# Kernel tuning notes

Hardware: AMD Instinct MI355X
Metric: run time of the kernel (lower is better)

The kernel has to match this reference:

```python
import jax, jax.numpy as jnp
import numpy as np

SOS_TOKEN = 0


def setup_inputs() -> dict:
    key = jax.random.key(0)
    ks = jax.random.split(key, 16)
    B, S, T, H, V = 64, 64, 32, 512, 32000
    s = 1.0 / np.sqrt(H)
    inp = {
        "encoder_outputs": jax.random.normal(ks[0], (B, S, H), jnp.float32),
        "encoder_hidden": jax.random.normal(ks[1], (1, B, H), jnp.float32),
        "target_tensor": jax.random.randint(ks[2], (B, T), 0, V),
        "emb": jax.random.normal(ks[3], (V, H), jnp.float32),
        "Wa": jax.random.uniform(ks[4], (H, H), jnp.float32, -s, s),
        "ba": jnp.zeros((H,), jnp.float32),
        "Ua": jax.random.uniform(ks[5], (H, H), jnp.float32, -s, s),
        "bu": jnp.zeros((H,), jnp.float32),
        "va": jax.random.uniform(ks[6], (H, 1), jnp.float32, -s, s),
        "bv": jnp.zeros((1,), jnp.float32),
        "w_ih": jax.random.uniform(ks[7], (3 * H, 2 * H), jnp.float32, -s, s),
        "b_ih": jax.random.uniform(ks[8], (3 * H,), jnp.float32, -s, s),
        "w_hh": jax.random.uniform(ks[9], (3 * H, H), jnp.float32, -s, s),
        "b_hh": jax.random.uniform(ks[10], (3 * H,), jnp.float32, -s, s),
        "Wo": jax.random.uniform(ks[11], (V, H), jnp.float32, -s, s),
        "bo": jax.random.uniform(ks[12], (V,), jnp.float32, -s, s),
    }
    return inp


def _gru_cell(x, h, w_ih, b_ih, w_hh, b_hh):
    # x: [B, 2H], h: [B, H] -- PyTorch nn.GRU gate math
    H = h.shape[-1]
    gi = x @ w_ih.T + b_ih            # [B, 3H]
    gh = h @ w_hh.T + b_hh            # [B, 3H]
    i_r, i_z, i_n = gi[:, :H], gi[:, H:2 * H], gi[:, 2 * H:]
    h_r, h_z, h_n = gh[:, :H], gh[:, H:2 * H], gh[:, 2 * H:]
    r = jax.nn.sigmoid(i_r + h_r)
    z = jax.nn.sigmoid(i_z + h_z)
    n = jnp.tanh(i_n + r * h_n)
    return (1.0 - z) * n + z * h


def reference(encoder_outputs, encoder_hidden, target_tensor,
              emb, Wa, ba, Ua, bu, va, bv,
              w_ih, b_ih, w_hh, b_hh, Wo, bo):
    B, S, H = encoder_outputs.shape
    T = target_tensor.shape[1]
    # Teacher forcing: step t input is SOS for t=0 else target[:, t-1]
    sos = jnp.full((B, 1), SOS_TOKEN, dtype=target_tensor.dtype)
    input_ids = jnp.concatenate([sos, target_tensor[:, :-1]], axis=1)  # [B, T]
    embedded = emb[input_ids]  # [B, T, H]  (dropout is identity in eval)

    # Precompute key projection once (invariant across steps)
    Ua_keys = encoder_outputs @ Ua.T + bu  # [B, S, H]

    def step(h, x_emb):
        # Bahdanau additive attention: query = hidden state
        scores = jnp.tanh(h[:, None, :] @ Wa.T + ba + Ua_keys) @ va + bv  # [B, S, 1]
        scores = scores[..., 0]                                           # [B, S]
        attn = jax.nn.softmax(scores, axis=-1)
        context = jnp.einsum('bs,bsh->bh', attn, encoder_outputs)
        x = jnp.concatenate([x_emb, context], axis=-1)                    # [B, 2H]
        h_new = _gru_cell(x, h, w_ih, b_ih, w_hh, b_hh)
        logits = h_new @ Wo.T + bo                                        # [B, V]
        return h_new, (logits, attn)

    h0 = encoder_hidden[0]  # [B, H]
    h_final, (logits_t, attn_t) = jax.lax.scan(step, h0, jnp.swapaxes(embedded, 0, 1))
    logits = jnp.swapaxes(logits_t, 0, 1)        # [B, T, V]
    attentions = jnp.swapaxes(attn_t, 0, 1)      # [B, T, S]
    log_probs = jax.nn.log_softmax(logits, axis=-1)
    decoder_hidden = h_final[None]               # [1, B, H]
    return (log_probs, decoder_hidden, attentions)
```

## Files before the change

kernel.cpp:

```cpp
#include <hip/hip_runtime.h>

typedef unsigned short u16;
typedef __bf16 bf16x8 __attribute__((ext_vector_type(8)));
typedef float f32x4 __attribute__((ext_vector_type(4)));

#define Bsz 64
#define Ssz 64
#define Tsz 32
#define Hsz 512
#define Vsz 32000
#define NCONV 160
#define NTOT 256

static __device__ inline u16 f2bf(float f) {
    union { float f; unsigned u; } v; v.f = f;
    unsigned u = v.u;
    unsigned r = (u + 0x7FFFu + ((u >> 16) & 1u)) >> 16;
    return (u16)r;
}
static __device__ inline float bf2f(u16 v) {
    union { unsigned u; float f; } x; x.u = ((unsigned)v) << 16; return x.f;
}
static __device__ inline float tanh_fast(float x) {
    float e = __expf(2.f * x);
    return 1.f - 2.f / (e + 1.f);
}
static __device__ inline void st_u32(unsigned* p, unsigned v) {
    __hip_atomic_store(p, v, __ATOMIC_RELAXED, __HIP_MEMORY_SCOPE_AGENT);
}
static __device__ inline unsigned ld_u32(const unsigned* p) {
    return __hip_atomic_load(p, __ATOMIC_RELAXED, __HIP_MEMORY_SCOPE_AGENT);
}

#define GLOAD_LDS16(g, l) \
    __builtin_amdgcn_global_load_lds((const __attribute__((address_space(1))) void*)(g), \
                                     (__attribute__((address_space(3))) void*)(l), 16, 0, 0)

__global__ void prep_kernel(const float* __restrict__ enc, const float* __restrict__ Ua,
                            const float* __restrict__ Wa, const float* __restrict__ wih,
                            const float* __restrict__ whh, const float* __restrict__ ehid,
                            u16* __restrict__ encbf, u16* __restrict__ Uabf,
                            u16* __restrict__ Wabf, u16* __restrict__ wihbf,
                            u16* __restrict__ whhbf, u16* __restrict__ h0bf) {
    const int n0 = 2097152, n1 = 262144, n2 = 262144, n3 = 1572864, n4 = 786432, n5 = 32768;
    const int total = n0 + n1 + n2 + n3 + n4 + n5;
    for (int i = blockIdx.x * blockDim.x + threadIdx.x; i < total; i += gridDim.x * blockDim.x) {
        int j = i;
        if (j < n0) { encbf[j] = f2bf(enc[j]); continue; } j -= n0;
        if (j < n1) { Uabf[j] = f2bf(Ua[j]); continue; } j -= n1;
        if (j < n2) { Wabf[j] = f2bf(Wa[j]); continue; } j -= n2;
        if (j < n3) { wihbf[j] = f2bf(wih[j]); continue; } j -= n3;
        if (j < n4) { whhbf[j] = f2bf(whh[j]); continue; } j -= n4;
        h0bf[j] = f2bf(ehid[j]);
    }
}

__global__ void embed_kernel(const int* __restrict__ target, const float* __restrict__ emb,
                             u16* __restrict__ xbuf) {
    int n = Tsz * Bsz * Hsz;
    for (int i = blockIdx.x * blockDim.x + threadIdx.x; i < n; i += gridDim.x * blockDim.x) {
        int t = i / (Bsz * Hsz);
        int rem = i % (Bsz * Hsz);
        int b = rem / Hsz, k = rem % Hsz;
        int id = (t == 0) ? 0 : target[b * Tsz + (t - 1)];
        xbuf[((size_t)t * Bsz + b) * 1024 + k] = f2bf(emb[(size_t)id * Hsz + k]);
    }
}

__global__ __launch_bounds__(256) void gemm_bt(const u16* __restrict__ A, const u16* __restrict__ Bw,
                                               const float* __restrict__ bias, float* __restrict__ out,
                                               int M, int N, int K) {
    __shared__ __align__(16) u16 As[128 * 32];
    __shared__ __align__(16) u16 Bs[128 * 32];
    int m0 = blockIdx.x * 128, n0 = blockIdx.y * 128;
    int tid = threadIdx.x, lane = tid & 63, wid = tid >> 6;
    int wm = wid & 1, wn = wid >> 1;
    f32x4 acc[4][4] = {};
    for (int k0 = 0; k0 < K; k0 += 32) {
        int e0 = wid * 64 + lane;
        int e1 = e0 + 256;
        GLOAD_LDS16(&A[(size_t)(m0 + (e0 >> 2)) * K + k0 + (e0 & 3) * 8], (char*)As + wid * 1024);
        GLOAD_LDS16(&A[(size_t)(m0 + (e1 >> 2)) * K + k0 + (e1 & 3) * 8], (char*)As + 4096 + wid * 1024);
        GLOAD_LDS16(&Bw[(size_t)(n0 + (e0 >> 2)) * K + k0 + (e0 & 3) * 8], (char*)Bs + wid * 1024);
        GLOAD_LDS16(&Bw[(size_t)(n0 + (e1 >> 2)) * K + k0 + (e1 & 3) * 8], (char*)Bs + 4096 + wid * 1024);
        __syncthreads();
        bf16x8 av[4], bvv[4];
        for (int mi = 0; mi < 4; ++mi)
            av[mi] = *(const bf16x8*)&As[(wm * 64 + mi * 16 + (lane & 15)) * 32 + (lane >> 4) * 8];
        for (int ni = 0; ni < 4; ++ni)
            bvv[ni] = *(const bf16x8*)&Bs[(wn * 64 + ni * 16 + (lane & 15)) * 32 + (lane >> 4) * 8];
        for (int mi = 0; mi < 4; ++mi)
            for (int ni = 0; ni < 4; ++ni)
                acc[mi][ni] = __builtin_amdgcn_mfma_f32_16x16x32_bf16(av[mi], bvv[ni], acc[mi][ni], 0, 0, 0);
        __syncthreads();
    }
    for (int mi = 0; mi < 4; ++mi)
        for (int ni = 0; ni < 4; ++ni) {
            int n = n0 + wn * 64 + ni * 16 + (lane & 15);
            float bb = bias[n];
            for (int r = 0; r < 4; ++r) {
                int m = m0 + wm * 64 + mi * 16 + (lane >> 4) * 4 + r;
                out[(size_t)m * N + n] = acc[mi][ni][r] + bb;
            }
        }
}

static __device__ inline void arrive(unsigned* bar, int slot, unsigned val, int tid) {
    asm volatile("s_waitcnt vmcnt(0)" ::: "memory");
    __syncthreads();
    if (tid == 0) st_u32(&bar[slot * 32], val);
}
static __device__ inline void pollflags(unsigned* bar, int base, int n, unsigned target, int tid) {
    if (tid < n) {
        unsigned* p = &bar[(base + tid) * 32];
        while (ld_u32(p) < target) {}
    }
    __syncthreads();
}

__global__ __launch_bounds__(512, 1) void coop_kernel(
    const float* __restrict__ uak,
    u16* __restrict__ xbuf, u16* __restrict__ Abf,
    const u16* __restrict__ h0bf, const u16* __restrict__ wihbf, const u16* __restrict__ whhbf,
    const u16* __restrict__ Wabf, const float* __restrict__ enc,
    const float* __restrict__ va, const float* __restrict__ bv, const float* __restrict__ ba,
    const float* __restrict__ b_ih, const float* __restrict__ b_hh,
    const float* __restrict__ ehid,
    const float* __restrict__ Wo, u16* __restrict__ Wobf,
    float* __restrict__ out, u16* __restrict__ partials,
    unsigned* __restrict__ bar) {
    __shared__ __align__(16) char lds[149504];
    __shared__ float WhL[512];
    __shared__ float scL[64];
    __shared__ float vaL[512];

    const size_t HID_OFF = (size_t)Bsz * Tsz * Vsz;
    const size_t ATT_OFF = HID_OFF + (size_t)Bsz * Hsz;

    int tid = threadIdx.x, lane = tid & 63, wid = tid >> 6;
    int ln15 = lane & 15, hi = lane >> 4;
    int bx = blockIdx.x;

    unsigned* xbufU = (unsigned*)xbuf;
    unsigned* AbfU = (unsigned*)Abf;
    unsigned* partU = (unsigned*)partials;

    if (bx < 64) {
        int b = bx;
        u16* uakL = (u16*)lds;
        u16* encL = (u16*)(lds + 65536);
        for (int i = tid; i < Ssz * Hsz; i += 512) {
            uakL[i] = f2bf(uak[(size_t)b * Ssz * Hsz + i]);
            encL[i] = f2bf(enc[(size_t)b * Ssz * Hsz + i]);
        }
        vaL[tid] = va[tid];
        float bvv = bv[0];
        float ba_t = ba[tid];
        int halfsel = tid & 1;
        __syncthreads();

        for (int t = 0; t < Tsz; ++t) {
            pollflags(bar, 64, 32, (unsigned)(t + 1), tid);
            {
                float acc = ba_t;
                const unsigned* pb = partU + (size_t)b * 256 + (tid >> 1);
#pragma unroll
                for (int g = 0; g < 32; ++g) {
                    unsigned pw = ld_u32(pb + (size_t)g * 16384);
                    acc += bf2f((u16)(halfsel ? (pw >> 16) : (pw & 0xffff)));
                }
                WhL[tid] = acc;
            }
            __syncthreads();
            for (int si = 0; si < 8; ++si) {
                int s = wid * 8 + si;
                float a = 0.f;
#pragma unroll
                for (int ji = 0; ji < 8; ++ji) {
                    int j = lane + ji * 64;
                    float x = WhL[j] + bf2f(uakL[s * 512 + j]);
                    a += tanh_fast(x) * vaL[j];
                }
                for (int off = 32; off; off >>= 1) a += __shfl_down(a, off);
                if (lane == 0) scL[s] = a + bvv;
            }
            __syncthreads();
            if (wid == 0) {
                float x = scL[lane];
                float mx = x;
                for (int off = 32; off; off >>= 1) mx = fmaxf(mx, __shfl_xor(mx, off));
                float e = __expf(x - mx);
                float sm = e;
                for (int off = 32; off; off >>= 1) sm += __shfl_xor(sm, off);
                float at = e / sm;
                scL[lane] = at;
                out[ATT_OFF + ((size_t)b * Tsz + t) * Ssz + lane] = at;
            }
            __syncthreads();
            float c = 0.f;
            for (int s = 0; s < Ssz; ++s)
                c += scL[s] * bf2f(encL[s * 512 + tid]);
            unsigned me = (unsigned)f2bf(c);
            unsigned other = __shfl_xor(me, 1);
            if ((tid & 1) == 0)
                st_u32(&xbufU[((size_t)t * Bsz + b) * 512 + 256 + (tid >> 1)], me | (other << 16));
            arrive(bar, bx, (unsigned)(t + 1), tid);
        }
    } else if (bx < 96) {
        int g = bx - 64, jbase = g * 16;
        u16* hsl = (u16*)(lds + 147456);
        for (int i = tid; i < 6144; i += 512) {
            int row = i >> 7, c16 = i & 127;
            int Rg = (row >> 4) * 512 + jbase + (row & 15);
            uint4 v = *(const uint4*)&wihbf[(size_t)Rg * 1024 + c16 * 8];
            *(uint4*)(lds + row * 2048 + ((c16 * 16) ^ ((row & 7) << 4))) = v;
        }
        for (int i = tid; i < 3072; i += 512) {
            int row = i >> 6, c16 = i & 63;
            int Rg = (row >> 4) * 512 + jbase + (row & 15);
            uint4 v = *(const uint4*)&whhbf[(size_t)Rg * 512 + c16 * 8];
            *(uint4*)(lds + 98304 + row * 1024 + ((c16 * 16) ^ ((row & 7) << 4))) = v;
        }
        const char* wih_l = lds;
        const char* whh_l = lds + 98304;
        int j = jbase + ln15;
        float bir = b_ih[j] + b_hh[j];
        float biz = b_ih[512 + j] + b_hh[512 + j];
        float bin = b_ih[1024 + j];
        float bhn = b_hh[1024 + j];
        float hp0 = 0.f, hp1 = 0.f, hp2 = 0.f, hp3 = 0.f;
        if (wid < 4) {
            int m = wid;
            hp0 = ehid[(size_t)(m * 16 + hi * 4 + 0) * Hsz + j];
            hp1 = ehid[(size_t)(m * 16 + hi * 4 + 1) * Hsz + j];
            hp2 = ehid[(size_t)(m * 16 + hi * 4 + 2) * Hsz + j];
            hp3 = ehid[(size_t)(m * 16 + hi * 4 + 3) * Hsz + j];
        }
        int swz = (ln15 & 7) << 4;
        bf16x8 zfr = {};
        bf16x8 wfrag[4];
#pragma unroll
        for (int i = 0; i < 4; ++i) {
            int jp = (wid * 4 + i) * 16 + ln15;
            wfrag[i] = (hi < 2) ? *(const bf16x8*)&Wabf[(size_t)jp * 512 + jbase + hi * 8] : zfr;
        }
        for (int i = tid; i < 1024; i += 512)
            hsl[i] = h0bf[(size_t)(i >> 4) * 512 + jbase + (i & 15)];
        __syncthreads();
#pragma unroll
        for (int mt = 0; mt < 4; ++mt) {
            bf16x8 af = (hi < 2) ? *(const bf16x8*)&hsl[(mt * 16 + ln15) * 16 + hi * 8] : zfr;
#pragma unroll
            for (int i = 0; i < 4; ++i) {
                f32x4 pacc = {};
                pacc = __builtin_amdgcn_mfma_f32_16x16x32_bf16(af, wfrag[i], pacc, 0, 0, 0);
                int n0 = (wid * 4 + i) * 16;
#pragma unroll
                for (int r = 0; r < 4; ++r) {
                    int b = mt * 16 + hi * 4 + r;
                    unsigned me = (unsigned)f2bf(pacc[r]);
                    unsigned other = __shfl_xor(me, 1);
                    if ((ln15 & 1) == 0)
                        st_u32(&partU[((size_t)g * 64 + b) * 256 + ((n0 + ln15) >> 1)], me | (other << 16));
                }
            }
        }
        arrive(bar, bx, 1u, tid);

        for (int t = 0; t < Tsz; ++t) {
            const u16* hbt = t ? (Abf + (size_t)(t - 1) * Bsz * Hsz) : h0bf;
            pollflags(bar, 64, 32, (unsigned)(t + 1), tid);
            f32x4 ar = {}, az = {}, ain = {}, ahn = {};
            if (wid < 4) {
                int m = wid;
#pragma unroll 8
                for (int k0 = 0; k0 < 16; ++k0) {
                    bf16x8 a = *(const bf16x8*)&xbuf[((size_t)t * Bsz + m * 16 + ln15) * 1024 + k0 * 32 + hi * 8];
                    int byteIn = k0 * 64 + hi * 16;
                    bf16x8 b0 = *(const bf16x8*)(wih_l + (0 + ln15) * 2048 + (byteIn ^ swz));
                    bf16x8 b1 = *(const bf16x8*)(wih_l + (16 + ln15) * 2048 + (byteIn ^ swz));
                    bf16x8 b2 = *(const bf16x8*)(wih_l + (32 + ln15) * 2048 + (byteIn ^ swz));
                    ar = __builtin_amdgcn_mfma_f32_16x16x32_bf16(a, b0, ar, 0, 0, 0);
                    az = __builtin_amdgcn_mfma_f32_16x16x32_bf16(a, b1, az, 0, 0, 0);
                    ain = __builtin_amdgcn_mfma_f32_16x16x32_bf16(a, b2, ain, 0, 0, 0);
                }
#pragma unroll 8
                for (int k0 = 0; k0 < 16; ++k0) {
                    bf16x8 a = *(const bf16x8*)&hbt[(size_t)(m * 16 + ln15) * 512 + k0 * 32 + hi * 8];
                    int byteIn = k0 * 64 + hi * 16;
                    bf16x8 b0 = *(const bf16x8*)(whh_l + (0 + ln15) * 1024 + (byteIn ^ swz));
                    bf16x8 b1 = *(const bf16x8*)(whh_l + (16 + ln15) * 1024 + (byteIn ^ swz));
                    bf16x8 b2 = *(const bf16x8*)(whh_l + (32 + ln15) * 1024 + (byteIn ^ swz));
                    ar = __builtin_amdgcn_mfma_f32_16x16x32_bf16(a, b0, ar, 0, 0, 0);
                    az = __builtin_amdgcn_mfma_f32_16x16x32_bf16(a, b1, az, 0, 0, 0);
                    ahn = __builtin_amdgcn_mfma_f32_16x16x32_bf16(a, b2, ahn, 0, 0, 0);
                }
                unsigned* p = &bar[(wid * 16 + ln15) * 32];
                while (ld_u32(p) < (unsigned)(t + 1)) {}
#pragma unroll 8
                for (int k0 = 16; k0 < 32; ++k0) {
                    bf16x8 a = *(const bf16x8*)&xbuf[((size_t)t * Bsz + m * 16 + ln15) * 1024 + k0 * 32 + hi * 8];
                    int byteIn = k0 * 64 + hi * 16;
                    bf16x8 b0 = *(const bf16x8*)(wih_l + (0 + ln15) * 2048 + (byteIn ^ swz));
                    bf16x8 b1 = *(const bf16x8*)(wih_l + (16 + ln15) * 2048 + (byteIn ^ swz));
                    bf16x8 b2 = *(const bf16x8*)(wih_l + (32 + ln15) * 2048 + (byteIn ^ swz));
                    ar = __builtin_amdgcn_mfma_f32_16x16x32_bf16(a, b0, ar, 0, 0, 0);
                    az = __builtin_amdgcn_mfma_f32_16x16x32_bf16(a, b1, az, 0, 0, 0);
                    ain = __builtin_amdgcn_mfma_f32_16x16x32_bf16(a, b2, ain, 0, 0, 0);
                }
                float hpv[4] = {hp0, hp1, hp2, hp3};
#pragma unroll
                for (int r = 0; r < 4; ++r) {
                    int b = m * 16 + hi * 4 + r;
                    float rg = 1.f / (1.f + __expf(-(ar[r] + bir)));
                    float zg = 1.f / (1.f + __expf(-(az[r] + biz)));
                    float ng = tanh_fast(ain[r] + bin + rg * (ahn[r] + bhn));
                    float hv = (1.f - zg) * ng + zg * hpv[r];
                    hpv[r] = hv;
                    u16 hb = f2bf(hv);
                    unsigned me = (unsigned)hb;
                    unsigned other = __shfl_xor(me, 1);
                    if ((ln15 & 1) == 0)
                        st_u32(&AbfU[((size_t)t * Bsz + b) * 256 + (j >> 1)], me | (other << 16));
                    hsl[b * 16 + ln15] = hb;
                    if (t == Tsz - 1) out[HID_OFF + (size_t)b * 512 + j] = hv;
                }
                hp0 = hpv[0]; hp1 = hpv[1]; hp2 = hpv[2]; hp3 = hpv[3];
            }
            __syncthreads();
#pragma unroll
            for (int mt = 0; mt < 4; ++mt) {
                bf16x8 af = (hi < 2) ? *(const bf16x8*)&hsl[(mt * 16 + ln15) * 16 + hi * 8] : zfr;
#pragma unroll
                for (int i = 0; i < 4; ++i) {
                    f32x4 pacc = {};
                    pacc = __builtin_amdgcn_mfma_f32_16x16x32_bf16(af, wfrag[i], pacc, 0, 0, 0);
                    int n0 = (wid * 4 + i) * 16;
#pragma unroll
                    for (int r = 0; r < 4; ++r) {
                        int b = mt * 16 + hi * 4 + r;
                        unsigned me = (unsigned)f2bf(pacc[r]);
                        unsigned other = __shfl_xor(me, 1);
                        if ((ln15 & 1) == 0)
                            st_u32(&partU[((size_t)g * 64 + b) * 256 + ((n0 + ln15) >> 1)], me | (other << 16));
                    }
                }
            }
            arrive(bar, bx, (unsigned)(t + 2), tid);
        }
    } else {
        const float4* W4 = (const float4*)Wo;
        for (int i = (bx - 96) * 512 + tid; i < (Vsz * Hsz) / 4; i += NCONV * 512) {
            float4 v = W4[i];
            ushort4 o;
            o.x = f2bf(v.x); o.y = f2bf(v.y); o.z = f2bf(v.z); o.w = f2bf(v.w);
            *(ushort4*)&Wobf[(size_t)i * 4] = o;
        }
    }
}

static __device__ inline void l_stage(const u16* __restrict__ Abf, const u16* __restrict__ Wobf,
                                      int m0, int n0, int k0, char* As, char* Bs, int wid, int lane) {
    int e0 = wid * 64 + lane;
    int r = e0 >> 2, c8 = (e0 & 3) * 8;
    GLOAD_LDS16(&Abf[(size_t)(m0 + r) * 512 + k0 + c8], As + wid * 1024);
    GLOAD_LDS16(&Wobf[(size_t)(n0 + r) * 512 + k0 + c8], Bs + wid * 1024);
    GLOAD_LDS16(&Wobf[(size_t)(n0 + 128 + r) * 512 + k0 + c8], Bs + 8192 + wid * 1024);
}

__global__ __launch_bounds__(512) void gemm_logits(const u16* __restrict__ Abf, const u16* __restrict__ Wobf,
                                                   const float* __restrict__ bo, float* __restrict__ out,
                                                   float* __restrict__ sumexp) {
    __shared__ __align__(16) char lds[49152];
    char* As0 = lds;
    char* Bs0 = lds + 8192;
    char* As1 = lds + 24576;
    char* Bs1 = lds + 32768;
    int tid = threadIdx.x, lane = tid & 63, wid = tid >> 6;
    int ln15 = lane & 15, hi = lane >> 4;
    int wm = wid & 1, wn = wid >> 1;
    int job = blockIdx.x;
    int m0 = (job / 125) * 128, n0 = (job % 125) * 256;
    f32x4 acc[4][4] = {};
    l_stage(Abf, Wobf, m0, n0, 0, As0, Bs0, wid, lane);
#pragma unroll 2
    for (int ks = 0; ks < 16; ++ks) {
        const u16* As = (const u16*)((ks & 1) ? As1 : As0);
        const u16* Bs = (const u16*)((ks & 1) ? Bs1 : Bs0);
        if (ks < 15) {
            l_stage(Abf, Wobf, m0, n0, (ks + 1) * 32,
                    (ks & 1) ? As0 : As1, (ks & 1) ? Bs0 : Bs1, wid, lane);
            asm volatile("s_waitcnt vmcnt(3)" ::: "memory");
        } else {
            asm volatile("s_waitcnt vmcnt(0)" ::: "memory");
        }
        __builtin_amdgcn_s_barrier();
        bf16x8 av[4], bvv[4];
        for (int mi = 0; mi < 4; ++mi)
            av[mi] = *(const bf16x8*)&As[(wm * 64 + mi * 16 + ln15) * 32 + hi * 8];
        for (int ni = 0; ni < 4; ++ni)
            bvv[ni] = *(const bf16x8*)&Bs[(wn * 64 + ni * 16 + ln15) * 32 + hi * 8];
        for (int mi = 0; mi < 4; ++mi)
            for (int ni = 0; ni < 4; ++ni)
                acc[mi][ni] = __builtin_amdgcn_mfma_f32_16x16x32_bf16(av[mi], bvv[ni], acc[mi][ni], 0, 0, 0);
        asm volatile("s_waitcnt lgkmcnt(0)" ::: "memory");
        __builtin_amdgcn_s_barrier();
    }
    float rowpart[4][4];
    for (int mi = 0; mi < 4; ++mi)
        for (int r = 0; r < 4; ++r) rowpart[mi][r] = 0.f;
    for (int mi = 0; mi < 4; ++mi)
        for (int ni = 0; ni < 4; ++ni) {
            int n = n0 + wn * 64 + ni * 16 + ln15;
            float bb = bo[n];
            for (int r = 0; r < 4; ++r) {
                int m = m0 + wm * 64 + mi * 16 + hi * 4 + r;
                int t = m >> 6, b = m & 63;
                float val = acc[mi][ni][r] + bb;
                out[((size_t)(b * Tsz + t)) * Vsz + n] = val;
                rowpart[mi][r] += __expf(val);
            }
        }
    for (int mi = 0; mi < 4; ++mi)
        for (int r = 0; r < 4; ++r) {
            float v = rowpart[mi][r];
            v += __shfl_xor(v, 1);
            v += __shfl_xor(v, 2);
            v += __shfl_xor(v, 4);
            v += __shfl_xor(v, 8);
            if (ln15 == 0) {
                int m = m0 + wm * 64 + mi * 16 + hi * 4 + r;
                atomicAdd(&sumexp[(m & 63) * Tsz + (m >> 6)], v);
            }
        }
}

__global__ void sub_kernel(float* __restrict__ out, const float* __restrict__ sumexp) {
    const int total4 = (Bsz * Tsz * Vsz) / 4;
    float4* o4 = (float4*)out;
    for (int i = blockIdx.x * blockDim.x + threadIdx.x; i < total4; i += gridDim.x * blockDim.x) {
        float l = __logf(sumexp[i / (Vsz / 4)]);
        float4 v = o4[i];
        v.x -= l; v.y -= l; v.z -= l; v.w -= l;
        o4[i] = v;
    }
}

extern "C" void kernel_launch(void* const* d_in, const int* in_sizes, int n_in,
                              void* d_out, int out_size, void* d_ws, size_t ws_size,
                              hipStream_t stream) {
    const float* enc   = (const float*)d_in[0];
    const float* ehid  = (const float*)d_in[1];
    const int*   target= (const int*)d_in[2];
    const float* emb   = (const float*)d_in[3];
    const float* Wa    = (const float*)d_in[4];
    const float* ba    = (const float*)d_in[5];
    const float* Ua    = (const float*)d_in[6];
    const float* bu    = (const float*)d_in[7];
    const float* va    = (const float*)d_in[8];
    const float* bv    = (const float*)d_in[9];
    const float* w_ih  = (const float*)d_in[10];
    const float* b_ih  = (const float*)d_in[11];
    const float* w_hh  = (const float*)d_in[12];
    const float* b_hh  = (const float*)d_in[13];
    const float* Wo    = (const float*)d_in[14];
    const float* bo    = (const float*)d_in[15];
    float* out = (float*)d_out;

    char* w = (char*)d_ws;
    float* uak    = (float*)w; w += (size_t)4096 * 512 * 4;
    float* sumexp = (float*)w; w += 8192;
    unsigned* bar = (unsigned*)w; w += 96 * 128;
    u16* xbuf     = (u16*)w;   w += (size_t)Tsz * Bsz * 1024 * 2;
    u16* Abf      = (u16*)w;   w += (size_t)Tsz * Bsz * Hsz * 2;
    u16* h0bf     = (u16*)w;   w += (size_t)Bsz * Hsz * 2;
    u16* partials = (u16*)w;   w += (size_t)32 * Bsz * Hsz * 2;
    u16* Wabf     = (u16*)w;   w += (size_t)Hsz * Hsz * 2;
    u16* encbf    = (u16*)w;   w += (size_t)4096 * 512 * 2;
    u16* Uabf     = (u16*)w;   w += (size_t)Hsz * Hsz * 2;
    u16* wihbf    = (u16*)w;   w += (size_t)1536 * 1024 * 2;
    u16* whhbf    = (u16*)w;   w += (size_t)1536 * 512 * 2;
    u16* Wobf     = (u16*)w;   w += (size_t)Vsz * 512 * 2;

    prep_kernel<<<2048, 256, 0, stream>>>(enc, Ua, Wa, w_ih, w_hh, ehid,
                                          encbf, Uabf, Wabf, wihbf, whhbf, h0bf);
    embed_kernel<<<1024, 256, 0, stream>>>(target, emb, xbuf);

    gemm_bt<<<dim3(32, 4), 256, 0, stream>>>(encbf, Uabf, bu, uak, 4096, 512, 512);

    hipMemsetAsync(bar, 0, 96 * 128, stream);
    hipMemsetAsync(sumexp, 0, 2048 * 4, stream);

    coop_kernel<<<NTOT, 512, 0, stream>>>(uak, xbuf, Abf, h0bf, wihbf, whhbf,
                                          Wabf, enc, va, bv, ba, b_ih, b_hh,
                                          ehid, Wo, Wobf, out, partials, bar);

    gemm_logits<<<2000, 512, 0, stream>>>(Abf, Wobf, bo, out, sumexp);

    sub_kernel<<<2048, 256, 0, stream>>>(out, sumexp);
}
```

Baseline: 976.4 us.

## Fuse embed into prep, sleep in spin-waits, move poll, coalesce logits epilogue

Folds the embedding gather into the prep conversion kernel to drop one launch. Adds s_sleep to spin-wait loops, which cuts memory traffic from polling. Moves the barrier poll in the GRU blocks after the input-side MFMAs so that work overlaps the wait. Rewrites the logits epilogue to stage each tile through LDS, giving coalesced float4 stores and one wavefront reduction per row for the sum of exponentials. The sleep can add wake-up latency on the critical recurrent path.

After: 844.9 us. 1.16x faster.

```diff
diff --git a/kernel.cpp b/kernel.cpp
--- a/kernel.cpp
+++ b/kernel.cpp
@@ -39,11 +39,14 @@
 __global__ void prep_kernel(const float* __restrict__ enc, const float* __restrict__ Ua,
                             const float* __restrict__ Wa, const float* __restrict__ wih,
                             const float* __restrict__ whh, const float* __restrict__ ehid,
+                            const int* __restrict__ target, const float* __restrict__ emb,
                             u16* __restrict__ encbf, u16* __restrict__ Uabf,
                             u16* __restrict__ Wabf, u16* __restrict__ wihbf,
-                            u16* __restrict__ whhbf, u16* __restrict__ h0bf) {
+                            u16* __restrict__ whhbf, u16* __restrict__ h0bf,
+                            u16* __restrict__ xbuf) {
     const int n0 = 2097152, n1 = 262144, n2 = 262144, n3 = 1572864, n4 = 786432, n5 = 32768;
-    const int total = n0 + n1 + n2 + n3 + n4 + n5;
+    const int n6 = Tsz * Bsz * Hsz;
+    const int total = n0 + n1 + n2 + n3 + n4 + n5 + n6;
     for (int i = blockIdx.x * blockDim.x + threadIdx.x; i < total; i += gridDim.x * blockDim.x) {
         int j = i;
         if (j < n0) { encbf[j] = f2bf(enc[j]); continue; } j -= n0;
@@ -51,19 +54,14 @@
         if (j < n2) { Wabf[j] = f2bf(Wa[j]); continue; } j -= n2;
         if (j < n3) { wihbf[j] = f2bf(wih[j]); continue; } j -= n3;
         if (j < n4) { whhbf[j] = f2bf(whh[j]); continue; } j -= n4;
-        h0bf[j] = f2bf(ehid[j]);
-    }
-}
-
-__global__ void embed_kernel(const int* __restrict__ target, const float* __restrict__ emb,
-                             u16* __restrict__ xbuf) {
-    int n = Tsz * Bsz * Hsz;
-    for (int i = blockIdx.x * blockDim.x + threadIdx.x; i < n; i += gridDim.x * blockDim.x) {
-        int t = i / (Bsz * Hsz);
-        int rem = i % (Bsz * Hsz);
-        int b = rem / Hsz, k = rem % Hsz;
-        int id = (t == 0) ? 0 : target[b * Tsz + (t - 1)];
-        xbuf[((size_t)t * Bsz + b) * 1024 + k] = f2bf(emb[(size_t)id * Hsz + k]);
+        if (j < n5) { h0bf[j] = f2bf(ehid[j]); continue; } j -= n5;
+        {
+            int t = j / (Bsz * Hsz);
+            int rem = j % (Bsz * Hsz);
+            int b = rem / Hsz, k = rem % Hsz;
+            int id = (t == 0) ? 0 : target[b * Tsz + (t - 1)];
+            xbuf[((size_t)t * Bsz + b) * 1024 + k] = f2bf(emb[(size_t)id * Hsz + k]);
+        }
     }
 }
 
@@ -110,10 +108,10 @@
     __syncthreads();
     if (tid == 0) st_u32(&bar[slot * 32], val);
 }
-static __device__ inline void pollflags(unsigned* bar, int base, int n, unsigned target, int tid) {
+static __device__ inline void pollflags1(unsigned* bar, int base, int n, unsigned target, int tid) {
     if (tid < n) {
         unsigned* p = &bar[(base + tid) * 32];
-        while (ld_u32(p) < target) {}
+        while (ld_u32(p) < target) asm volatile("s_sleep 1");
     }
     __syncthreads();
 }
@@ -160,7 +158,7 @@
         __syncthreads();
 
         for (int t = 0; t < Tsz; ++t) {
-            pollflags(bar, 64, 32, (unsigned)(t + 1), tid);
+            pollflags1(bar, 64, 32, (unsigned)(t + 1), tid);
             {
                 float acc = ba_t;
                 const unsigned* pb = partU + (size_t)b * 256 + (tid >> 1);
@@ -269,7 +267,6 @@
 
         for (int t = 0; t < Tsz; ++t) {
             const u16* hbt = t ? (Abf + (size_t)(t - 1) * Bsz * Hsz) : h0bf;
-            pollflags(bar, 64, 32, (unsigned)(t + 1), tid);
             f32x4 ar = {}, az = {}, ain = {}, ahn = {};
             if (wid < 4) {
                 int m = wid;
@@ -284,6 +281,10 @@
                     az = __builtin_amdgcn_mfma_f32_16x16x32_bf16(a, b1, az, 0, 0, 0);
                     ain = __builtin_amdgcn_mfma_f32_16x16x32_bf16(a, b2, ain, 0, 0, 0);
                 }
+            }
+            pollflags1(bar, 64, 32, (unsigned)(t + 1), tid);
+            if (wid < 4) {
+                int m = wid;
 #pragma unroll 8
                 for (int k0 = 0; k0 < 16; ++k0) {
                     bf16x8 a = *(const bf16x8*)&hbt[(size_t)(m * 16 + ln15) * 512 + k0 * 32 + hi * 8];
@@ -296,7 +297,7 @@
                     ahn = __builtin_amdgcn_mfma_f32_16x16x32_bf16(a, b2, ahn, 0, 0, 0);
                 }
                 unsigned* p = &bar[(wid * 16 + ln15) * 32];
-                while (ld_u32(p) < (unsigned)(t + 1)) {}
+                while (ld_u32(p) < (unsigned)(t + 1)) asm volatile("s_sleep 1");
 #pragma unroll 8
                 for (int k0 = 16; k0 < 32; ++k0) {
                     bf16x8 a = *(const bf16x8*)&xbuf[((size_t)t * Bsz + m * 16 + ln15) * 1024 + k0 * 32 + hi * 8];
@@ -359,15 +360,6 @@
     }
 }
 
-static __device__ inline void l_stage(const u16* __restrict__ Abf, const u16* __restrict__ Wobf,
-                                      int m0, int n0, int k0, char* As, char* Bs, int wid, int lane) {
-    int e0 = wid * 64 + lane;
-    int r = e0 >> 2, c8 = (e0 & 3) * 8;
-    GLOAD_LDS16(&Abf[(size_t)(m0 + r) * 512 + k0 + c8], As + wid * 1024);
-    GLOAD_LDS16(&Wobf[(size_t)(n0 + r) * 512 + k0 + c8], Bs + wid * 1024);
-    GLOAD_LDS16(&Wobf[(size_t)(n0 + 128 + r) * 512 + k0 + c8], Bs + 8192 + wid * 1024);
-}
-
 __global__ __launch_bounds__(512) void gemm_logits(const u16* __restrict__ Abf, const u16* __restrict__ Wobf,
                                                    const float* __restrict__ bo, float* __restrict__ out,
                                                    float* __restrict__ sumexp) {
@@ -382,14 +374,24 @@
     int job = blockIdx.x;
     int m0 = (job / 125) * 128, n0 = (job % 125) * 256;
     f32x4 acc[4][4] = {};
-    l_stage(Abf, Wobf, m0, n0, 0, As0, Bs0, wid, lane);
+    {
+        int e0 = wid * 64 + lane, r = e0 >> 2, c8 = (e0 & 3) * 8;
+        GLOAD_LDS16(&Abf[(size_t)(m0 + r) * 512 + c8], As0 + wid * 1024);
+        GLOAD_LDS16(&Wobf[(size_t)(n0 + r) * 512 + c8], Bs0 + wid * 1024);
+        GLOAD_LDS16(&Wobf[(size_t)(n0 + 128 + r) * 512 + c8], Bs0 + 8192 + wid * 1024);
+    }
 #pragma unroll 2
     for (int ks = 0; ks < 16; ++ks) {
         const u16* As = (const u16*)((ks & 1) ? As1 : As0);
         const u16* Bs = (const u16*)((ks & 1) ? Bs1 : Bs0);
         if (ks < 15) {
-            l_stage(Abf, Wobf, m0, n0, (ks + 1) * 32,
-                    (ks & 1) ? As0 : As1, (ks & 1) ? Bs0 : Bs1, wid, lane);
+            char* Asn = (ks & 1) ? As0 : As1;
+            char* Bsn = (ks & 1) ? Bs0 : Bs1;
+            int e0 = wid * 64 + lane, r = e0 >> 2, c8 = (e0 & 3) * 8;
+            int k0 = (ks + 1) * 32;
+            GLOAD_LDS16(&Abf[(size_t)(m0 + r) * 512 + k0 + c8], Asn + wid * 1024);
+            GLOAD_LDS16(&Wobf[(size_t)(n0 + r) * 512 + k0 + c8], Bsn + wid * 1024);
+            GLOAD_LDS16(&Wobf[(size_t)(n0 + 128 + r) * 512 + k0 + c8], Bsn + 8192 + wid * 1024);
             asm volatile("s_waitcnt vmcnt(3)" ::: "memory");
         } else {
             asm volatile("s_waitcnt vmcnt(0)" ::: "memory");
@@ -406,33 +408,31 @@
         asm volatile("s_waitcnt lgkmcnt(0)" ::: "memory");
         __builtin_amdgcn_s_barrier();
     }
-    float rowpart[4][4];
-    for (int mi = 0; mi < 4; ++mi)
-        for (int r = 0; r < 4; ++r) rowpart[mi][r] = 0.f;
-    for (int mi = 0; mi < 4; ++mi)
-        for (int ni = 0; ni < 4; ++ni) {
-            int n = n0 + wn * 64 + ni * 16 + ln15;
-            float bb = bo[n];
-            for (int r = 0; r < 4; ++r) {
-                int m = m0 + wm * 64 + mi * 16 + hi * 4 + r;
-                int t = m >> 6, b = m & 63;
-                float val = acc[mi][ni][r] + bb;
-                out[((size_t)(b * Tsz + t)) * Vsz + n] = val;
-                rowpart[mi][r] += __expf(val);
-            }
-        }
-    for (int mi = 0; mi < 4; ++mi)
-        for (int r = 0; r < 4; ++r) {
-            float v = rowpart[mi][r];
-            v += __shfl_xor(v, 1);
-            v += __shfl_xor(v, 2);
-            v += __shfl_xor(v, 4);
-            v += __shfl_xor(v, 8);
-            if (ln15 == 0) {
-                int m = m0 + wm * 64 + mi * 16 + hi * 4 + r;
-                atomicAdd(&sumexp[(m & 63) * Tsz + (m >> 6)], v);
-            }
-        }
+    float* eps = (float*)lds;
+    float bb[4];
+#pragma unroll
+    for (int ni = 0; ni < 4; ++ni) bb[ni] = bo[n0 + wn * 64 + ni * 16 + ln15];
+    for (int mi = 0; mi < 4; ++mi) {
+        __syncthreads();
+#pragma unroll
+        for (int ni = 0; ni < 4; ++ni)
+#pragma unroll
+            for (int r = 0; r < 4; ++r)
+                eps[(wm * 16 + hi * 4 + r) * 256 + wn * 64 + ni * 16 + ln15] = acc[mi][ni][r] + bb[ni];
+        __syncthreads();
+#pragma unroll
+        for (int k = 0; k < 4; ++k) {
+            int idx = k * 512 + tid;
+            int l = idx >> 6, c4 = idx & 63;
+            int m = m0 + (l >> 4) * 64 + mi * 16 + (l & 15);
+            int t = m >> 6, b = m & 63;
+            float4 v = *(float4*)&eps[l * 256 + c4 * 4];
+            *(float4*)&out[((size_t)(b * Tsz + t)) * Vsz + n0 + c4 * 4] = v;
+            float e = __expf(v.x) + __expf(v.y) + __expf(v.z) + __expf(v.w);
+            for (int off = 32; off; off >>= 1) e += __shfl_down(e, off);
+            if (lane == 0) atomicAdd(&sumexp[(m & 63) * Tsz + (m >> 6)], e);
+        }
+    }
 }
 
 __global__ void sub_kernel(float* __restrict__ out, const float* __restrict__ sumexp) {
@@ -470,7 +470,7 @@
     char* w = (char*)d_ws;
     float* uak    = (float*)w; w += (size_t)4096 * 512 * 4;
     float* sumexp = (float*)w; w += 8192;
-    unsigned* bar = (unsigned*)w; w += 96 * 128;
+    unsigned* bar = (unsigned*)w; w += 128 * 128;
     u16* xbuf     = (u16*)w;   w += (size_t)Tsz * Bsz * 1024 * 2;
     u16* Abf      = (u16*)w;   w += (size_t)Tsz * Bsz * Hsz * 2;
     u16* h0bf     = (u16*)w;   w += (size_t)Bsz * Hsz * 2;
@@ -482,13 +482,12 @@
     u16* whhbf    = (u16*)w;   w += (size_t)1536 * 512 * 2;
     u16* Wobf     = (u16*)w;   w += (size_t)Vsz * 512 * 2;
 
-    prep_kernel<<<2048, 256, 0, stream>>>(enc, Ua, Wa, w_ih, w_hh, ehid,
-                                          encbf, Uabf, Wabf, wihbf, whhbf, h0bf);
-    embed_kernel<<<1024, 256, 0, stream>>>(target, emb, xbuf);
+    prep_kernel<<<2048, 256, 0, stream>>>(enc, Ua, Wa, w_ih, w_hh, ehid, target, emb,
+                                          encbf, Uabf, Wabf, wihbf, whhbf, h0bf, xbuf);
 
     gemm_bt<<<dim3(32, 4), 256, 0, stream>>>(encbf, Uabf, bu, uak, 4096, 512, 512);
 
-    hipMemsetAsync(bar, 0, 96 * 128, stream);
+    hipMemsetAsync(bar, 0, 128 * 128, stream);
     hipMemsetAsync(sumexp, 0, 2048 * 4, stream);
 
     coop_kernel<<<NTOT, 512, 0, stream>>>(uak, xbuf, Abf, h0bf, wihbf, whhbf,
```
